# Kernel optimization log

Measured on AMD Instinct MI355X. Metric: run time of the kernel, lower is better.

The kernel has to match this reference:

```python
import jax, jax.numpy as jnp
import numpy as np

B, K, P, T = 4096, 128, 64, 4

def setup_inputs() -> dict:
    key = jax.random.key(0)
    ks = jax.random.split(key, 9)
    s = lambda k, shp: jax.random.normal(k, shp, dtype=jnp.float32) * 0.1
    return {
        "x": jax.random.normal(ks[0], (B, K, 1), dtype=jnp.float32),
        "w": jax.random.normal(ks[1], (B, K, 1), dtype=jnp.float32),
        "W1": s(ks[2], (P, 1)),   # theta_1: 1 -> p
        "W2": s(ks[3], (P, P)),   # theta_2: p -> p
        "W3": s(ks[4], (P, P)),   # theta_3: p -> p
        "W4": s(ks[5], (P, 1)),   # theta_4: 1 -> p
        "W5": s(ks[6], (1, 2 * P)),  # theta_5: 2p -> 1
        "W6": s(ks[7], (P, P)),   # theta_6: p -> p
        "W7": s(ks[8], (P, P)),   # theta_7: p -> p
    }


def reference(x, w, W1, W2, W3, W4, W5, W6, W7):
    # x, w: (B, K, 1). torch Linear(in,out,bias=False): y = v @ W.T, W: (out,in)
    b, k, _ = x.shape
    p = W1.shape[0]
    # per-node feature messages (invariant across T iterations in original code)
    tmsg = jax.nn.relu(jnp.einsum('bki,pi->bkp', w, W4))   # relu(theta_4(w_k)), (B,K,p)
    sum_t = tmsg.sum(axis=1, keepdims=True)                # (B,1,p)
    xmsg = jnp.einsum('bki,pi->bkp', x, W1)                # theta_1(x_k), (B,K,p)
    mu = jnp.zeros((b, k, p), dtype=x.dtype)
    for _ in range(T):
        sum_mu = mu.sum(axis=1, keepdims=True)             # (B,1,p)
        mu = jax.nn.relu(
            xmsg
            + jnp.einsum('bkp,qp->bkq', sum_mu - mu, W2)   # theta_2(sum_mu - mu_k)
            + jnp.einsum('bkp,qp->bkq', sum_t - tmsg, W3)  # theta_3(sum_t - t_k)
        )
    pooled = jax.nn.relu(jnp.einsum('bp,qp->bq', mu.sum(axis=1), W6))  # (B,p)
    local = jnp.einsum('bkp,qp->bkq', mu, W7)                           # (B,K,p)
    # theta_5(concat(relu(theta_6(pool)), theta_7(mu_k))); split W5 = [W5a | W5b]
    W5a, W5b = W5[:, :p], W5[:, p:]
    q = jnp.einsum('bp,op->bo', pooled, W5a)[:, None, :] + jnp.einsum('bkp,op->bko', local, W5b)
    return q  # (B, K, 1)
```

## Files before the change

kernel.cpp:

```cpp
#include <hip/hip_runtime.h>

typedef __bf16 bf16;
typedef __bf16 bf16x4 __attribute__((ext_vector_type(4)));
typedef __bf16 bf16x8 __attribute__((ext_vector_type(8)));
typedef float  f32x4  __attribute__((ext_vector_type(4)));

#define MFMA16(a, b, c) __builtin_amdgcn_mfma_f32_16x16x32_bf16((a), (b), (c), 0, 0, 0)

__global__ __launch_bounds__(64, 2)
void qnet_kernel(const float* __restrict__ Xg, const float* __restrict__ Wg,
                 const float* __restrict__ W1g, const float* __restrict__ W2g,
                 const float* __restrict__ W3g, const float* __restrict__ W4g,
                 const float* __restrict__ W5g, const float* __restrict__ W6g,
                 const float* __restrict__ W7g, float* __restrict__ Outg)
{
    __shared__ __align__(16) bf16 muS[128 * 72];
    __shared__ __align__(16) float uS[64];
    __shared__ __align__(16) float smS[64];

    const int lane = threadIdx.x;
    const int b    = blockIdx.x;
    const int l15  = lane & 15;
    const int quad = lane >> 4;

    float xv0 = Xg[b * 128 + lane], xv1 = Xg[b * 128 + 64 + lane];
    float wv0 = Wg[b * 128 + lane], wv1 = Wg[b * 128 + 64 + lane];

    float Ap = fmaxf(wv0, 0.f) + fmaxf(wv1, 0.f);
    float Bn = fmaxf(-wv0, 0.f) + fmaxf(-wv1, 0.f);
#pragma unroll
    for (int m = 1; m < 64; m <<= 1) { Ap += __shfl_xor(Ap, m); Bn += __shfl_xor(Bn, m); }

    float xk[8], apk[8], bnk[8];
#pragma unroll
    for (int kt = 0; kt < 8; ++kt) {
        const int src = (kt & 3) * 16 + l15;
        float xs_ = (kt < 4) ? __shfl(xv0, src) : __shfl(xv1, src);
        float ws_ = (kt < 4) ? __shfl(wv0, src) : __shfl(wv1, src);
        xk[kt]  = xs_;
        apk[kt] = Ap - fmaxf(ws_, 0.f);
        bnk[kt] = Bn - fmaxf(-ws_, 0.f);
    }

    float sp = 0.f, sm = 0.f;
#pragma unroll
    for (int c = 0; c < 16; ++c) {
        f32x4 w4 = *(const f32x4*)&W4g[c * 4];
        f32x4 w3 = *(const f32x4*)&W3g[lane * 64 + c * 4];
#pragma unroll
        for (int e = 0; e < 4; ++e) {
            sp += fmaxf(w4[e], 0.f) * w3[e];
            sm += fmaxf(-w4[e], 0.f) * w3[e];
        }
    }
    float v3pC[16], v3mC[16], w1C[16];
#pragma unroll
    for (int qt = 0; qt < 4; ++qt) {
        f32x4 w1v = *(const f32x4*)&W1g[qt * 16 + quad * 4];
#pragma unroll
        for (int e = 0; e < 4; ++e) {
            const int q = qt * 16 + quad * 4 + e;
            v3pC[qt * 4 + e] = __shfl(sp, q);
            v3mC[qt * 4 + e] = __shfl(sm, q);
            w1C[qt * 4 + e]  = w1v[e];
        }
    }

    bf16x8 w2h[4][2], w2l[4][2];
#pragma unroll
    for (int qt = 0; qt < 4; ++qt)
#pragma unroll
        for (int s = 0; s < 2; ++s) {
            const float* src = &W2g[(qt * 16 + l15) * 64 + s * 32 + quad * 8];
            f32x4 f0 = *(const f32x4*)src;
            f32x4 f1 = *(const f32x4*)(src + 4);
            bf16x8 h, l;
#pragma unroll
            for (int e = 0; e < 4; ++e) {
                bf16 h0 = (bf16)f0[e], h1 = (bf16)f1[e];
                h[e] = h0; h[4 + e] = h1;
                l[e]     = (bf16)(f0[e] - (float)h0);
                l[4 + e] = (bf16)(f1[e] - (float)h1);
            }
            w2h[qt][s] = h; w2l[qt][s] = l;
        }

    {
        float u = 0.f;
#pragma unroll
        for (int c = 0; c < 16; ++c) {
            f32x4 w5v = *(const f32x4*)&W5g[64 + c * 4];
#pragma unroll
            for (int e = 0; e < 4; ++e)
                u += w5v[e] * W7g[(c * 4 + e) * 64 + lane];
        }
        uS[lane] = u;
    }

#pragma unroll
    for (int kt = 0; kt < 8; ++kt) {
        const int row = (kt * 16 + l15) * 72;
#pragma unroll
        for (int qt = 0; qt < 4; ++qt) {
            bf16x4 h;
#pragma unroll
            for (int e = 0; e < 4; ++e) {
                float t = fmaf(xk[kt], w1C[qt * 4 + e],
                          fmaf(apk[kt], v3pC[qt * 4 + e], bnk[kt] * v3mC[qt * 4 + e]));
                h[e] = (bf16)fmaxf(t, 0.f);
            }
            *(bf16x4*)&muS[row + qt * 16 + quad * 4] = h;
        }
    }

    const f32x4 zero4 = {0.f, 0.f, 0.f, 0.f};
    float smv[16];
#pragma unroll
    for (int i = 0; i < 16; ++i) smv[i] = 0.f;

    for (int it = 0; it < 3; ++it) {
        f32x4 rs[4] = {zero4, zero4, zero4, zero4};
#pragma unroll
        for (int kt = 0; kt < 8; ++kt) {
            const int row = (kt * 16 + l15) * 72;
            bf16x8 m0 = *(bf16x8*)&muS[row + quad * 8];
            bf16x8 m1 = *(bf16x8*)&muS[row + 32 + quad * 8];
#pragma unroll
            for (int qt = 0; qt < 4; ++qt) {
                f32x4 a = MFMA16(w2h[qt][0], m0, zero4);
                a = MFMA16(w2h[qt][1], m1, a);
                a = MFMA16(w2l[qt][0], m0, a);
                a = MFMA16(w2l[qt][1], m1, a);
                rs[qt] += a;
            }
        }
#pragma unroll
        for (int m = 1; m <= 8; m <<= 1)
#pragma unroll
            for (int qt = 0; qt < 4; ++qt)
#pragma unroll
                for (int e = 0; e < 4; ++e)
                    rs[qt][e] += __shfl_xor(rs[qt][e], m);

#pragma unroll
        for (int kt = 0; kt < 8; ++kt) {
            const int row = (kt * 16 + l15) * 72;
            bf16x8 m0 = *(bf16x8*)&muS[row + quad * 8];
            bf16x8 m1 = *(bf16x8*)&muS[row + 32 + quad * 8];
#pragma unroll
            for (int qt = 0; qt < 4; ++qt) {
                f32x4 a = MFMA16(w2h[qt][0], m0, zero4);
                a = MFMA16(w2h[qt][1], m1, a);
                bf16x4 h;
#pragma unroll
                for (int e = 0; e < 4; ++e) {
                    float t = fmaf(xk[kt], w1C[qt * 4 + e], rs[qt][e]);
                    t = fmaf(apk[kt], v3pC[qt * 4 + e], t);
                    t = fmaf(bnk[kt], v3mC[qt * 4 + e], t);
                    float v = fmaxf(t - a[e], 0.f);
                    h[e] = (bf16)v;
                    if (it == 2) smv[qt * 4 + e] += v;
                }
                *(bf16x4*)&muS[row + qt * 16 + quad * 4] = h;
            }
        }
    }

#pragma unroll
    for (int m = 1; m <= 8; m <<= 1)
#pragma unroll
        for (int i = 0; i < 16; ++i) smv[i] += __shfl_xor(smv[i], m);
    if (l15 == 0) {
#pragma unroll
        for (int qt = 0; qt < 4; ++qt) {
            f32x4 v = {smv[qt * 4 + 0], smv[qt * 4 + 1], smv[qt * 4 + 2], smv[qt * 4 + 3]};
            *(f32x4*)&smS[qt * 16 + quad * 4] = v;
        }
    }

    float pl = 0.f;
#pragma unroll
    for (int c = 0; c < 16; ++c) {
        f32x4 sv  = *(const f32x4*)&smS[c * 4];
        f32x4 w6v = *(const f32x4*)&W6g[lane * 64 + c * 4];
#pragma unroll
        for (int e = 0; e < 4; ++e) pl += sv[e] * w6v[e];
    }
    float qa = fmaxf(pl, 0.f) * W5g[lane];
#pragma unroll
    for (int m = 1; m < 64; m <<= 1) qa += __shfl_xor(qa, m);

#pragma unroll
    for (int h2 = 0; h2 < 2; ++h2) {
        const int k = lane + 64 * h2;
        float accq = qa;
#pragma unroll
        for (int j = 0; j < 8; ++j) {
            bf16x8 m8 = *(bf16x8*)&muS[k * 72 + j * 8];
            f32x4 u0 = *(const f32x4*)&uS[j * 8];
            f32x4 u1 = *(const f32x4*)&uS[j * 8 + 4];
#pragma unroll
            for (int e = 0; e < 4; ++e) accq += (float)m8[e] * u0[e];
#pragma unroll
            for (int e = 0; e < 4; ++e) accq += (float)m8[4 + e] * u1[e];
        }
        Outg[b * 128 + k] = accq;
    }
}

extern "C" void kernel_launch(void* const* d_in, const int* in_sizes, int n_in,
                              void* d_out, int out_size, void* d_ws, size_t ws_size,
                              hipStream_t stream) {
    (void)n_in; (void)d_ws; (void)ws_size; (void)out_size;
    const int B = in_sizes[0] >> 7;
    qnet_kernel<<<B, 64, 0, stream>>>(
        (const float*)d_in[0], (const float*)d_in[1], (const float*)d_in[2],
        (const float*)d_in[3], (const float*)d_in[4], (const float*)d_in[5],
        (const float*)d_in[6], (const float*)d_in[7], (const float*)d_in[8],
        (float*)d_out);
}
```

Baseline: 138.4 us.

## Compute column-sum term via fp32 matvec, drop split-bf16 MFMA pass and swizzle LDS

The per-iteration sum over nodes of W2·mu is replaced by summing mu in registers while it is written and then doing one fp32 64x64 matvec (W2·sum_mu) per iteration. This removes the first MFMA pass over all 128 rows and the hi/lo split weights. The mu tile in LDS loses its row padding and uses an XOR swizzle to avoid bank conflicts. The final output dot product is rewritten to use the swizzled layout with cross-lane reductions, and launch bounds are raised to allow three waves. The bf16 lo-correction term is dropped, so precision of the remaining W2·mu_k term relies on bf16 weights only.

```diff
diff --git a/kernel.cpp b/kernel.cpp
--- a/kernel.cpp
+++ b/kernel.cpp
@@ -7,21 +7,23 @@
 
 #define MFMA16(a, b, c) __builtin_amdgcn_mfma_f32_16x16x32_bf16((a), (b), (c), 0, 0, 0)
 
-__global__ __launch_bounds__(64, 2)
+__global__ __launch_bounds__(64, 3)
 void qnet_kernel(const float* __restrict__ Xg, const float* __restrict__ Wg,
                  const float* __restrict__ W1g, const float* __restrict__ W2g,
                  const float* __restrict__ W3g, const float* __restrict__ W4g,
                  const float* __restrict__ W5g, const float* __restrict__ W6g,
                  const float* __restrict__ W7g, float* __restrict__ Outg)
 {
-    __shared__ __align__(16) bf16 muS[128 * 72];
+    __shared__ __align__(16) bf16 muS[128 * 64];
     __shared__ __align__(16) float uS[64];
     __shared__ __align__(16) float smS[64];
+    __shared__ __align__(16) float s2S[64];
 
     const int lane = threadIdx.x;
     const int b    = blockIdx.x;
     const int l15  = lane & 15;
     const int quad = lane >> 4;
+    const int sw   = l15 & 7;
 
     float xv0 = Xg[b * 128 + lane], xv1 = Xg[b * 128 + 64 + lane];
     float wv0 = Wg[b * 128 + lane], wv1 = Wg[b * 128 + 64 + lane];
@@ -53,7 +55,7 @@
             sm += fmaxf(-w4[e], 0.f) * w3[e];
         }
     }
-    float v3pC[16], v3mC[16], w1C[16];
+    float w1C[16], v3pC[16], v3mC[16];
 #pragma unroll
     for (int qt = 0; qt < 4; ++qt) {
         f32x4 w1v = *(const f32x4*)&W1g[qt * 16 + quad * 4];
@@ -66,7 +68,18 @@
         }
     }
 
-    bf16x8 w2h[4][2], w2l[4][2];
+    {
+        float u = 0.f;
+#pragma unroll
+        for (int c = 0; c < 16; ++c) {
+            f32x4 w5v = *(const f32x4*)&W5g[64 + c * 4];
+#pragma unroll
+            for (int e = 0; e < 4; ++e) u += w5v[e] * W7g[(c * 4 + e) * 64 + lane];
+        }
+        uS[lane] = u;
+    }
+
+    bf16x8 w2h[4][2];
 #pragma unroll
     for (int qt = 0; qt < 4; ++qt)
 #pragma unroll
@@ -74,32 +87,18 @@
             const float* src = &W2g[(qt * 16 + l15) * 64 + s * 32 + quad * 8];
             f32x4 f0 = *(const f32x4*)src;
             f32x4 f1 = *(const f32x4*)(src + 4);
-            bf16x8 h, l;
-#pragma unroll
-            for (int e = 0; e < 4; ++e) {
-                bf16 h0 = (bf16)f0[e], h1 = (bf16)f1[e];
-                h[e] = h0; h[4 + e] = h1;
-                l[e]     = (bf16)(f0[e] - (float)h0);
-                l[4 + e] = (bf16)(f1[e] - (float)h1);
-            }
-            w2h[qt][s] = h; w2l[qt][s] = l;
-        }
-
-    {
-        float u = 0.f;
-#pragma unroll
-        for (int c = 0; c < 16; ++c) {
-            f32x4 w5v = *(const f32x4*)&W5g[64 + c * 4];
-#pragma unroll
-            for (int e = 0; e < 4; ++e)
-                u += w5v[e] * W7g[(c * 4 + e) * 64 + lane];
-        }
-        uS[lane] = u;
-    }
-
+            bf16x8 h;
+#pragma unroll
+            for (int e = 0; e < 4; ++e) { h[e] = (bf16)f0[e]; h[4 + e] = (bf16)f1[e]; }
+            w2h[qt][s] = h;
+        }
+
+    float smv[16];
+#pragma unroll
+    for (int i = 0; i < 16; ++i) smv[i] = 0.f;
 #pragma unroll
     for (int kt = 0; kt < 8; ++kt) {
-        const int row = (kt * 16 + l15) * 72;
+        const int k = kt * 16 + l15;
 #pragma unroll
         for (int qt = 0; qt < 4; ++qt) {
             bf16x4 h;
@@ -107,46 +106,49 @@
             for (int e = 0; e < 4; ++e) {
                 float t = fmaf(xk[kt], w1C[qt * 4 + e],
                           fmaf(apk[kt], v3pC[qt * 4 + e], bnk[kt] * v3mC[qt * 4 + e]));
-                h[e] = (bf16)fmaxf(t, 0.f);
-            }
-            *(bf16x4*)&muS[row + qt * 16 + quad * 4] = h;
+                float v = fmaxf(t, 0.f);
+                smv[qt * 4 + e] += v;
+                h[e] = (bf16)v;
+            }
+            *(bf16x4*)&muS[k * 64 + ((2 * qt + (quad >> 1)) ^ sw) * 8 + 4 * (quad & 1)] = h;
         }
     }
 
     const f32x4 zero4 = {0.f, 0.f, 0.f, 0.f};
-    float smv[16];
-#pragma unroll
-    for (int i = 0; i < 16; ++i) smv[i] = 0.f;
-
     for (int it = 0; it < 3; ++it) {
-        f32x4 rs[4] = {zero4, zero4, zero4, zero4};
+#pragma unroll
+        for (int m = 1; m <= 8; m <<= 1)
+#pragma unroll
+            for (int i = 0; i < 16; ++i) smv[i] += __shfl_xor(smv[i], m);
+        if (l15 == 0) {
+#pragma unroll
+            for (int qt = 0; qt < 4; ++qt) {
+                f32x4 v = {smv[qt * 4], smv[qt * 4 + 1], smv[qt * 4 + 2], smv[qt * 4 + 3]};
+                *(f32x4*)&smS[qt * 16 + quad * 4] = v;
+            }
+        }
+        {
+            float a0 = 0.f, a1 = 0.f, a2 = 0.f, a3 = 0.f;
+#pragma unroll
+            for (int c = 0; c < 16; ++c) {
+                f32x4 sv = *(const f32x4*)&smS[c * 4];
+                f32x4 wv = *(const f32x4*)&W2g[lane * 64 + c * 4];
+                a0 = fmaf(sv[0], wv[0], a0); a1 = fmaf(sv[1], wv[1], a1);
+                a2 = fmaf(sv[2], wv[2], a2); a3 = fmaf(sv[3], wv[3], a3);
+            }
+            s2S[lane] = (a0 + a1) + (a2 + a3);
+        }
+        f32x4 s2q[4];
+#pragma unroll
+        for (int qt = 0; qt < 4; ++qt) s2q[qt] = *(const f32x4*)&s2S[qt * 16 + quad * 4];
+
+#pragma unroll
+        for (int i = 0; i < 16; ++i) smv[i] = 0.f;
 #pragma unroll
         for (int kt = 0; kt < 8; ++kt) {
-            const int row = (kt * 16 + l15) * 72;
-            bf16x8 m0 = *(bf16x8*)&muS[row + quad * 8];
-            bf16x8 m1 = *(bf16x8*)&muS[row + 32 + quad * 8];
-#pragma unroll
-            for (int qt = 0; qt < 4; ++qt) {
-                f32x4 a = MFMA16(w2h[qt][0], m0, zero4);
-                a = MFMA16(w2h[qt][1], m1, a);
-                a = MFMA16(w2l[qt][0], m0, a);
-                a = MFMA16(w2l[qt][1], m1, a);
-                rs[qt] += a;
-            }
-        }
-#pragma unroll
-        for (int m = 1; m <= 8; m <<= 1)
-#pragma unroll
-            for (int qt = 0; qt < 4; ++qt)
-#pragma unroll
-                for (int e = 0; e < 4; ++e)
-                    rs[qt][e] += __shfl_xor(rs[qt][e], m);
-
-#pragma unroll
-        for (int kt = 0; kt < 8; ++kt) {
-            const int row = (kt * 16 + l15) * 72;
-            bf16x8 m0 = *(bf16x8*)&muS[row + quad * 8];
-            bf16x8 m1 = *(bf16x8*)&muS[row + 32 + quad * 8];
+            const int k = kt * 16 + l15;
+            bf16x8 m0 = *(const bf16x8*)&muS[k * 64 + ((quad) ^ sw) * 8];
+            bf16x8 m1 = *(const bf16x8*)&muS[k * 64 + ((4 + quad) ^ sw) * 8];
 #pragma unroll
             for (int qt = 0; qt < 4; ++qt) {
                 f32x4 a = MFMA16(w2h[qt][0], m0, zero4);
@@ -154,14 +156,13 @@
                 bf16x4 h;
 #pragma unroll
                 for (int e = 0; e < 4; ++e) {
-                    float t = fmaf(xk[kt], w1C[qt * 4 + e], rs[qt][e]);
-                    t = fmaf(apk[kt], v3pC[qt * 4 + e], t);
-                    t = fmaf(bnk[kt], v3mC[qt * 4 + e], t);
-                    float v = fmaxf(t - a[e], 0.f);
+                    float t = fmaf(xk[kt], w1C[qt * 4 + e],
+                              fmaf(apk[kt], v3pC[qt * 4 + e], bnk[kt] * v3mC[qt * 4 + e]));
+                    float v = fmaxf(t + s2q[qt][e] - a[e], 0.f);
+                    smv[qt * 4 + e] += v;
                     h[e] = (bf16)v;
-                    if (it == 2) smv[qt * 4 + e] += v;
                 }
-                *(bf16x4*)&muS[row + qt * 16 + quad * 4] = h;
+                *(bf16x4*)&muS[k * 64 + ((2 * qt + (quad >> 1)) ^ sw) * 8 + 4 * (quad & 1)] = h;
             }
         }
     }
@@ -173,7 +174,7 @@
     if (l15 == 0) {
 #pragma unroll
         for (int qt = 0; qt < 4; ++qt) {
-            f32x4 v = {smv[qt * 4 + 0], smv[qt * 4 + 1], smv[qt * 4 + 2], smv[qt * 4 + 3]};
+            f32x4 v = {smv[qt * 4], smv[qt * 4 + 1], smv[qt * 4 + 2], smv[qt * 4 + 3]};
             *(f32x4*)&smS[qt * 16 + quad * 4] = v;
         }
     }
@@ -181,31 +182,47 @@
     float pl = 0.f;
 #pragma unroll
     for (int c = 0; c < 16; ++c) {
-        f32x4 sv  = *(const f32x4*)&smS[c * 4];
-        f32x4 w6v = *(const f32x4*)&W6g[lane * 64 + c * 4];
-#pragma unroll
-        for (int e = 0; e < 4; ++e) pl += sv[e] * w6v[e];
+        f32x4 sv = *(const f32x4*)&smS[c * 4];
+        f32x4 w6 = *(const f32x4*)&W6g[lane * 64 + c * 4];
+#pragma unroll
+        for (int e = 0; e < 4; ++e) pl = fmaf(sv[e], w6[e], pl);
     }
     float qa = fmaxf(pl, 0.f) * W5g[lane];
 #pragma unroll
     for (int m = 1; m < 64; m <<= 1) qa += __shfl_xor(qa, m);
 
-#pragma unroll
-    for (int h2 = 0; h2 < 2; ++h2) {
-        const int k = lane + 64 * h2;
-        float accq = qa;
-#pragma unroll
-        for (int j = 0; j < 8; ++j) {
-            bf16x8 m8 = *(bf16x8*)&muS[k * 72 + j * 8];
-            f32x4 u0 = *(const f32x4*)&uS[j * 8];
-            f32x4 u1 = *(const f32x4*)&uS[j * 8 + 4];
-#pragma unroll
-            for (int e = 0; e < 4; ++e) accq += (float)m8[e] * u0[e];
-#pragma unroll
-            for (int e = 0; e < 4; ++e) accq += (float)m8[4 + e] * u1[e];
-        }
-        Outg[b * 128 + k] = accq;
-    }
+    f32x4 uf[2][2];
+#pragma unroll
+    for (int s = 0; s < 2; ++s) {
+        uf[s][0] = *(const f32x4*)&uS[s * 32 + quad * 8];
+        uf[s][1] = *(const f32x4*)&uS[s * 32 + quad * 8 + 4];
+    }
+
+    float res[8];
+#pragma unroll
+    for (int kt = 0; kt < 8; ++kt) {
+        const int k = kt * 16 + l15;
+        bf16x8 m0 = *(const bf16x8*)&muS[k * 64 + ((quad) ^ sw) * 8];
+        bf16x8 m1 = *(const bf16x8*)&muS[k * 64 + ((4 + quad) ^ sw) * 8];
+        float r = 0.f;
+#pragma unroll
+        for (int j = 0; j < 4; ++j) {
+            r = fmaf((float)m0[j],     uf[0][0][j], r);
+            r = fmaf((float)m0[4 + j], uf[0][1][j], r);
+            r = fmaf((float)m1[j],     uf[1][0][j], r);
+            r = fmaf((float)m1[4 + j], uf[1][1][j], r);
+        }
+        r += __shfl_xor(r, 16); r += __shfl_xor(r, 32);
+        res[kt] = r;
+    }
+    float rA0 = (quad & 1) ? res[1] : res[0];
+    float rA1 = (quad & 1) ? res[3] : res[2];
+    float rA  = (quad & 2) ? rA1 : rA0;
+    float rB0 = (quad & 1) ? res[5] : res[4];
+    float rB1 = (quad & 1) ? res[7] : res[6];
+    float rB  = (quad & 2) ? rB1 : rB0;
+    Outg[b * 128 + lane]      = qa + rA;
+    Outg[b * 128 + 64 + lane] = qa + rB;
 }
 
 extern "C" void kernel_launch(void* const* d_in, const int* in_sizes, int n_in,
```

After: 446.2 us. 222% more time.
